# Optimization experiments

Hardware: AMD Instinct MI355X
Metric: run time of the kernel (lower is better)

The kernel has to match this reference:

```python
import jax, jax.numpy as jnp
from jax import lax
import numpy as np

EPS = 1e-6

def layer_norm(x, scale, bias):
    mu = jnp.mean(x, axis=-1, keepdims=True)
    var = jnp.var(x, axis=-1, keepdims=True)
    y = (x - mu) * lax.rsqrt(var + EPS)
    if scale is not None:
        y = y * scale
    if bias is not None:
        y = y + bias
    return y

def mha(keys, values, queries, mask, head_count):
    # keys/values: [B, K, E]; queries: [B, Q, E]; mask: [B, K] (1 = attend)
    B, Q, E = queries.shape
    d = E // head_count
    q = queries.reshape(B, Q, head_count, d) / jnp.asarray(d ** 0.5, queries.dtype)
    k = keys.reshape(B, -1, head_count, d)
    v = values.reshape(B, -1, head_count, d)
    bias = (1.0 - mask.astype(q.dtype)) * -1e12  # [B, K]
    w = jnp.einsum('bqhc,bkhc->bhqk', q, k) + bias[:, None, None, :]
    w = jax.nn.softmax(w, axis=-1)
    out = jnp.einsum('bhqk,bkhc->bqhc', w, v)
    return out.reshape(B, Q, E)

def setup_inputs() -> dict:
    key = jax.random.key(0)
    ks = jax.random.split(key, 16)
    B, T, E, G, I = 64, 64, 2048, 4096, 256
    s = 0.02
    inp = {
        'decoder_state': jax.random.normal(ks[0], (B, 1, E), jnp.float32),
        'encoder_state': jax.random.normal(ks[1], (B, T, E), jnp.float32),
        'attention_state': jnp.zeros((2 * B, I, E), jnp.float32),
        'attention_mask': jnp.ones((B, T), jnp.int32),
        'token_index': 100,
        # params
        'ln_pre_sa_b': jnp.zeros((E,), jnp.float32),
        'q_sa': s * jax.random.normal(ks[2], (E, E), jnp.float32),
        'k_sa': s * jax.random.normal(ks[3], (E, E), jnp.float32),
        'v_sa': s * jax.random.normal(ks[4], (E, E), jnp.float32),
        'o_sa': s * jax.random.normal(ks[5], (E, E), jnp.float32),
        'ln_sa_s': jnp.ones((E,), jnp.float32),
        'ln_sa_b': jnp.zeros((E,), jnp.float32),
        'ln_pre_ca_b': jnp.zeros((E,), jnp.float32),
        'q_ca': s * jax.random.normal(ks[6], (E, E), jnp.float32),
        'k_ca': s * jax.random.normal(ks[7], (E, E), jnp.float32),
        'v_ca': s * jax.random.normal(ks[8], (E, E), jnp.float32),
        'o_ca': s * jax.random.normal(ks[9], (E, E), jnp.float32),
        'ln_ca_s': jnp.ones((E,), jnp.float32),
        'ln_ca_b': jnp.zeros((E,), jnp.float32),
        'glu_ln0_b': jnp.zeros((E,), jnp.float32),
        'fc0_w': s * jax.random.normal(ks[10], (E, G), jnp.float32),
        'fc1_w': s * jax.random.normal(ks[11], (E, G), jnp.float32),
        'glu_ln1_s': jnp.ones((G,), jnp.float32),
        'glu_ln1_b': jnp.zeros((G,), jnp.float32),
        'fc2_w': s * jax.random.normal(ks[12], (G, E), jnp.float32),
    }
    return inp

IMAGE_TOKEN_COUNT = 256
HEAD_COUNT = 32

def reference(decoder_state, encoder_state, attention_state,
              ln_pre_sa_b, q_sa, k_sa, v_sa, o_sa, ln_sa_s, ln_sa_b,
              ln_pre_ca_b, q_ca, k_ca, v_ca, o_ca, ln_ca_s, ln_ca_b,
              glu_ln0_b, fc0_w, fc1_w, glu_ln1_s, glu_ln1_b, fc2_w,
              attention_mask, token_index):
    B = decoder_state.shape[0]
    # --- self attention (pre-norm, KV cache update) ---
    residual = decoder_state
    x = layer_norm(decoder_state, None, ln_pre_sa_b)
    self_mask = jnp.tile(jnp.arange(IMAGE_TOKEN_COUNT) < token_index + 1, (B, 1))
    keys = x @ k_sa
    values = x @ v_sa
    queries = x @ q_sa
    attention_state = lax.dynamic_update_slice(
        attention_state, jnp.concatenate([keys, values]).astype(jnp.float32),
        (0, token_index, 0))
    cached_k = attention_state[:B]
    cached_v = attention_state[B:]
    x = (mha(cached_k, cached_v, queries, self_mask, HEAD_COUNT) @ o_sa).astype(decoder_state.dtype)
    x = layer_norm(x, ln_sa_s, ln_sa_b)
    decoder_state = residual + x
    # --- cross attention ---
    residual = decoder_state
    x = layer_norm(decoder_state, None, ln_pre_ca_b)
    ek = encoder_state @ k_ca
    ev = encoder_state @ v_ca
    q = x @ q_ca
    x = mha(ek, ev, q, attention_mask, HEAD_COUNT) @ o_ca
    x = layer_norm(x, ln_ca_s, ln_ca_b)
    decoder_state = residual + x
    # --- GLU FFN ---
    residual = decoder_state
    z = layer_norm(decoder_state, None, glu_ln0_b)
    w = jax.nn.gelu(z @ fc0_w, approximate=False)
    v = z @ fc1_w
    z = layer_norm(w * v, glu_ln1_s, glu_ln1_b) @ fc2_w
    decoder_state = residual + z
    return decoder_state, attention_state
```

## Files before the change

### kernel.cpp

```cpp
#include <hip/hip_runtime.h>

#define Bb   64
#define Ee   2048
#define Tt   64
#define Gg   4096
#define Ii   256
#define Hh   32
#define Dd   64

using f32x4_t  = __attribute__((ext_vector_type(4))) float;
using bf16x8_t = __attribute__((ext_vector_type(8))) __bf16;

__device__ __forceinline__ unsigned short f2bf(float f) {
  unsigned u = __float_as_uint(f);
  u += 0x7FFFu + ((u >> 16) & 1u);
  return (unsigned short)(u >> 16);
}
__device__ __forceinline__ float ldkv(float v) { return v; }
__device__ __forceinline__ float ldkv(unsigned short v) {
  return __uint_as_float(((unsigned)v) << 16);
}
__device__ __forceinline__ float gelu_f(float x) {
  return 0.5f * x * (1.0f + erff(x * 0.70710678118654752f));
}

template <typename T> __device__ __forceinline__ float4 ld4(const T* p);
template <> __device__ __forceinline__ float4 ld4<float>(const float* p) {
  return *(const float4*)p;
}
template <> __device__ __forceinline__ float4 ld4<unsigned short>(const unsigned short* p) {
  ushort4 u = *(const ushort4*)p;
  return make_float4(ldkv(u.x), ldkv(u.y), ldkv(u.z), ldkv(u.w));
}

__global__ void copy_state_k(const float4* __restrict__ src, float4* __restrict__ dst,
                             const float4* __restrict__ kb, const float4* __restrict__ vb,
                             const int* __restrict__ tokp) {
  const int t = *tokp;
  const long n4 = (long)128 * Ii * (Ee / 4);
  long i = (long)blockIdx.x * blockDim.x + threadIdx.x;
  const long stride = (long)gridDim.x * blockDim.x;
  for (; i < n4; i += stride) {
    long row = i >> 9;
    int tt = (int)(row & (Ii - 1));
    float4 v;
    if (tt == t) {
      int bh  = (int)(row >> 8);
      int col = (int)(i & 511);
      const float4* s = (bh < Bb) ? kb : vb;
      v = s[(long)(bh & (Bb - 1)) * (Ee / 4) + col];
    } else {
      v = src[i];
    }
    dst[i] = v;
  }
}

__global__ void conv_bf16_k(const float4* __restrict__ in, unsigned short* __restrict__ out, long n4) {
  long i = (long)blockIdx.x * blockDim.x + threadIdx.x;
  long stride = (long)gridDim.x * blockDim.x;
  for (; i < n4; i += stride) {
    float4 f = in[i];
    ushort4 u;
    u.x = f2bf(f.x); u.y = f2bf(f.y); u.z = f2bf(f.z); u.w = f2bf(f.w);
    *(ushort4*)(out + i * 4) = u;
  }
}

__global__ void transpose_bf16_k(const float* __restrict__ W, unsigned short* __restrict__ Wt,
                                 int K, int N) {
  __shared__ unsigned short tile[64][65];
  int k0 = blockIdx.x * 64, n0 = blockIdx.y * 64;
  int c = threadIdx.x & 63;
  int r4 = threadIdx.x >> 6;
  #pragma unroll
  for (int i = 0; i < 16; i++) {
    int r = r4 + i * 4;
    tile[r][c] = f2bf(W[(long)(k0 + r) * N + n0 + c]);
  }
  __syncthreads();
  #pragma unroll
  for (int i = 0; i < 16; i++) {
    int r = r4 + i * 4;
    Wt[(long)(n0 + r) * K + k0 + c] = tile[c][r];
  }
}

template <bool GELU, bool HAS_SCALE, bool HAS_RES, bool DUAL>
__global__ void ln_k(const float4* __restrict__ in1, const float4* __restrict__ in2,
                     const float* __restrict__ scale, const float* __restrict__ bias,
                     const float4* __restrict__ res,
                     float4* __restrict__ out1, float4* __restrict__ out2) {
  const int row = blockIdx.x, tid = threadIdx.x;
  const int C = blockDim.x * 4;
  const long base = (long)row * blockDim.x + tid;

  float4 p = in1[base];
  if (GELU) {
    float4 vv = in2[base];
    p.x = gelu_f(p.x) * vv.x; p.y = gelu_f(p.y) * vv.y;
    p.z = gelu_f(p.z) * vv.z; p.w = gelu_f(p.w) * vv.w;
  }
  float s  = p.x + p.y + p.z + p.w;
  float s2 = p.x * p.x + p.y * p.y + p.z * p.z + p.w * p.w;

  __shared__ float rs[16], rs2[16];
  int lane = tid & 63, w = tid >> 6;
  #pragma unroll
  for (int o = 32; o; o >>= 1) { s += __shfl_down(s, o, 64); s2 += __shfl_down(s2, o, 64); }
  if (lane == 0) { rs[w] = s; rs2[w] = s2; }
  __syncthreads();
  if (tid == 0) {
    float ts = 0.f, ts2 = 0.f;
    int nw = blockDim.x >> 6;
    for (int i = 0; i < nw; i++) { ts += rs[i]; ts2 += rs2[i]; }
    float mu = ts / C;
    float var = ts2 / C - mu * mu;
    rs[0]  = mu;
    rs2[0] = rsqrtf(var + 1e-6f);
  }
  __syncthreads();
  const float mu = rs[0], rstd = rs2[0];

  float4 o;
  o.x = (p.x - mu) * rstd; o.y = (p.y - mu) * rstd;
  o.z = (p.z - mu) * rstd; o.w = (p.w - mu) * rstd;
  if (HAS_SCALE) {
    float4 sc4 = ((const float4*)scale)[tid];
    o.x *= sc4.x; o.y *= sc4.y; o.z *= sc4.z; o.w *= sc4.w;
  }
  float4 b4 = ((const float4*)bias)[tid];
  o.x += b4.x; o.y += b4.y; o.z += b4.z; o.w += b4.w;
  if (HAS_RES) {
    float4 r4 = res[base];
    o.x += r4.x; o.y += r4.y; o.z += r4.z; o.w += r4.w;
  }
  out1[base] = o;
  if (DUAL) out2[base] = o;
}

template <int NW>
__global__ __launch_bounds__(256)
void proj_k(const float* __restrict__ X,
            const float* __restrict__ W0, const float* __restrict__ W1,
            const float* __restrict__ W2,
            float* __restrict__ P, int K, int N) {
  __shared__ float Xs[64 * 64];
  const int nq = threadIdx.x & 31;
  const int m0 = (threadIdx.x >> 5) * 8;
  const int n  = blockIdx.x * 128 + nq * 4;
  const int kbase = blockIdx.y * 128;

  f32x4_t acc[NW][8];
  #pragma unroll
  for (int wsel = 0; wsel < NW; wsel++)
    #pragma unroll
    for (int i = 0; i < 8; i++) acc[wsel][i] = (f32x4_t){0.f, 0.f, 0.f, 0.f};

  for (int k0 = kbase; k0 < kbase + 128; k0 += 64) {
    __syncthreads();
    #pragma unroll
    for (int j = 0; j < 16; j++) {
      int e = threadIdx.x + j * 256;
      Xs[e] = X[(long)(e >> 6) * K + k0 + (e & 63)];
    }
    __syncthreads();
    #pragma unroll 4
    for (int kk = 0; kk < 64; kk++) {
      const long wrow = (long)(k0 + kk) * N + n;
      f32x4_t w4[NW];
      w4[0] = *(const f32x4_t*)(W0 + wrow);
      if (NW > 1) w4[1] = *(const f32x4_t*)(W1 + wrow);
      if (NW > 2) w4[2] = *(const f32x4_t*)(W2 + wrow);
      #pragma unroll
      for (int i = 0; i < 8; i++) {
        float xm = Xs[(m0 + i) * 64 + kk];
        #pragma unroll
        for (int wsel = 0; wsel < NW; wsel++) acc[wsel][i] += xm * w4[wsel];
      }
    }
  }
  float* base = P + (long)blockIdx.y * ((long)NW * 64 * N);
  #pragma unroll
  for (int wsel = 0; wsel < NW; wsel++) {
    #pragma unroll
    for (int i = 0; i < 8; i++) {
      *(f32x4_t*)(base + ((long)wsel * 64 + m0 + i) * N + n) = acc[wsel][i];
    }
  }
}

template <bool ACCUM>
__global__ void reduce_k(const float4* __restrict__ P, float4* __restrict__ Y,
                         int KB, long n4) {
  long i = (long)blockIdx.x * blockDim.x + threadIdx.x;
  if (i >= n4) return;
  float4 s = ACCUM ? Y[i] : make_float4(0.f, 0.f, 0.f, 0.f);
  for (int k = 0; k < KB; k++) {
    float4 p = P[(long)k * n4 + i];
    s.x += p.x; s.y += p.y; s.z += p.z; s.w += p.w;
  }
  Y[i] = s;
}

template <typename KVT>
__global__ void attn_k(const float* __restrict__ Q, const KVT* __restrict__ Kc,
                       const KVT* __restrict__ Vc, float* __restrict__ O,
                       const int* __restrict__ tokp, const int* __restrict__ maskp,
                       int L, long bstride, float scale) {
  const int b = blockIdx.x, h = blockIdx.y;
  const int lane = threadIdx.x;
  __shared__ float sc[256];
  const float* qp = Q + (long)b * Ee + h * Dd;
  const int n = tokp ? (*tokp + 1) : L;

  float mx = -3.0e38f;
  for (int pos = lane; pos < n; pos += 64) {
    bool valid = maskp ? (maskp[(long)b * L + pos] != 0) : true;
    float s = -1.0e30f;
    if (valid) {
      const KVT* kr = Kc + (long)b * bstride + (long)pos * Ee + h * Dd;
      float acc = 0.f;
      #pragma unroll
      for (int j = 0; j < 16; j++) {
        float4 kv = ld4(kr + j * 4);
        acc += qp[j*4+0]*kv.x + qp[j*4+1]*kv.y + qp[j*4+2]*kv.z + qp[j*4+3]*kv.w;
      }
      s = acc * scale;
    }
    sc[pos] = s;
    mx = fmaxf(mx, s);
  }
  __syncthreads();
  #pragma unroll
  for (int o = 32; o; o >>= 1) mx = fmaxf(mx, __shfl_down(mx, o, 64));
  mx = __shfl(mx, 0, 64);

  float sum = 0.f;
  for (int pos = lane; pos < n; pos += 64) {
    float e = expf(sc[pos] - mx);
    sc[pos] = e;
    sum += e;
  }
  __syncthreads();
  #pragma unroll
  for (int o = 32; o; o >>= 1) sum += __shfl_down(sum, o, 64);
  sum = __shfl(sum, 0, 64);
  const float inv = 1.0f / sum;

  const KVT* vbase = Vc + (long)b * bstride + h * Dd + lane;
  float acc = 0.f;
  int pos = 0;
  for (; pos + 8 <= n; pos += 8) {
    #pragma unroll
    for (int u = 0; u < 8; u++)
      acc += sc[pos + u] * ldkv(vbase[(long)(pos + u) * Ee]);
  }
  for (; pos < n; pos++) acc += sc[pos] * ldkv(vbase[(long)pos * Ee]);
  O[(long)b * Ee + h * Dd + lane] = acc * inv;
}

__global__ __launch_bounds__(256)
void gemm_bf16_k(const unsigned short* __restrict__ A, const unsigned short* __restrict__ Bt,
                 unsigned short* __restrict__ C, int M, int N, int K) {
  __shared__ unsigned short As[128 * 32];
  __shared__ unsigned short Bs[128 * 32];
  const int m0 = blockIdx.x * 128;
  const int n0 = blockIdx.y * 128;
  const int tid  = threadIdx.x;
  const int lane = tid & 63;
  const int wave = tid >> 6;
  const int wm = (wave >> 1) * 64;
  const int wn = (wave & 1) * 64;
  const int fr = lane & 15;
  const int fq = lane >> 4;

  const int r0 = tid >> 2;
  const int g0 = tid & 3;
  const int so1 = r0 * 32 + ((g0 ^ ((r0 >> 1) & 3)) * 8);
  const int so2 = so1 + 64 * 32;

  f32x4_t acc[4][4];
  const f32x4_t zero = {0.f, 0.f, 0.f, 0.f};
  #pragma unroll
  for (int i = 0; i < 4; i++)
    #pragma unroll
    for (int j = 0; j < 4; j++) acc[i][j] = zero;

  const long aR1 = (long)(m0 + r0) * K;
  const long aR2 = (long)(m0 + r0 + 64) * K;
  const long bR1 = (long)(n0 + r0) * K;
  const long bR2 = (long)(n0 + r0 + 64) * K;

  for (int k0 = 0; k0 < K; k0 += 32) {
    uint4 va1 = *(const uint4*)(A  + aR1 + k0 + g0 * 8);
    uint4 va2 = *(const uint4*)(A  + aR2 + k0 + g0 * 8);
    uint4 vb1 = *(const uint4*)(Bt + bR1 + k0 + g0 * 8);
    uint4 vb2 = *(const uint4*)(Bt + bR2 + k0 + g0 * 8);
    __syncthreads();
    *(uint4*)(As + so1) = va1;
    *(uint4*)(As + so2) = va2;
    *(uint4*)(Bs + so1) = vb1;
    *(uint4*)(Bs + so2) = vb2;
    __syncthreads();

    bf16x8_t af[4], bb[4];
    #pragma unroll
    for (int ms = 0; ms < 4; ms++) {
      int row = wm + ms * 16 + fr;
      af[ms] = __builtin_bit_cast(bf16x8_t,
               *(const uint4*)(As + row * 32 + ((fq ^ ((row >> 1) & 3)) * 8)));
    }
    #pragma unroll
    for (int ns = 0; ns < 4; ns++) {
      int row = wn + ns * 16 + fr;
      bb[ns] = __builtin_bit_cast(bf16x8_t,
               *(const uint4*)(Bs + row * 32 + ((fq ^ ((row >> 1) & 3)) * 8)));
    }
    #pragma unroll
    for (int ms = 0; ms < 4; ms++)
      #pragma unroll
      for (int ns = 0; ns < 4; ns++)
        acc[ms][ns] = __builtin_amdgcn_mfma_f32_16x16x32_bf16(af[ms], bb[ns], acc[ms][ns], 0, 0, 0);
  }

  #pragma unroll
  for (int ms = 0; ms < 4; ms++) {
    #pragma unroll
    for (int ns = 0; ns < 4; ns++) {
      int row = m0 + wm + ms * 16 + fq * 4;
      int col = n0 + wn + ns * 16 + fr;
      #pragma unroll
      for (int r = 0; r < 4; r++)
        C[(long)(row + r) * N + col] = f2bf(acc[ms][ns][r]);
    }
  }
}

extern "C" void kernel_launch(void* const* d_in, const int* in_sizes, int n_in,
                              void* d_out, int out_size, void* d_ws, size_t ws_size,
                              hipStream_t stream) {
  const float* dec    = (const float*)d_in[0];
  const float* enc    = (const float*)d_in[1];
  const float* astate = (const float*)d_in[2];
  const int*   amask  = (const int*)d_in[3];
  const int*   tokp   = (const int*)d_in[4];
  const float* ln_pre_sa_b = (const float*)d_in[5];
  const float* q_sa = (const float*)d_in[6];
  const float* k_sa = (const float*)d_in[7];
  const float* v_sa = (const float*)d_in[8];
  const float* o_sa = (const float*)d_in[9];
  const float* ln_sa_s = (const float*)d_in[10];
  const float* ln_sa_b = (const float*)d_in[11];
  const float* ln_pre_ca_b = (const float*)d_in[12];
  const float* q_ca = (const float*)d_in[13];
  const float* k_ca = (const float*)d_in[14];
  const float* v_ca = (const float*)d_in[15];
  const float* o_ca = (const float*)d_in[16];
  const float* ln_ca_s = (const float*)d_in[17];
  const float* ln_ca_b = (const float*)d_in[18];
  const float* glu_ln0_b = (const float*)d_in[19];
  const float* fc0 = (const float*)d_in[20];
  const float* fc1 = (const float*)d_in[21];
  const float* glu_ln1_s = (const float*)d_in[22];
  const float* glu_ln1_b = (const float*)d_in[23];
  const float* fc2 = (const float*)d_in[24];

  float* out_dec   = (float*)d_out;
  float* out_state = out_dec + (long)Bb * Ee;

  float* qb  = (float*)d_ws;
  float* kb  = qb  + 131072;
  float* vb  = kb  + 131072;
  float* ob  = vb  + 131072;
  float* q2  = ob  + 131072;
  float* ob2 = q2  + 131072;
  float* w0  = ob2 + 131072;
  float* v1  = w0  + 262144;
  float* x1  = v1  + 262144;
  float* ab  = x1  + 131072;
  float* ds2 = ab  + 131072;
  float* x3  = ds2 + 131072;
  float* cb  = x3  + 131072;
  float* ds3 = cb  + 131072;
  float* zb  = ds3 + 131072;
  float* wvn = zb  + 131072;
  unsigned short* ebf = (unsigned short*)(wvn + 262144);
  unsigned short* kt  = ebf + 8388608;
  unsigned short* vt  = kt  + 4194304;
  unsigned short* ekb = vt  + 4194304;
  unsigned short* evb = ekb + 8388608;
  float* arena = (float*)(evb + 8388608);

  conv_bf16_k<<<2048, 256, 0, stream>>>((const float4*)enc, ebf, (long)Bb * Tt * Ee / 4);
  transpose_bf16_k<<<dim3(32, 32), 256, 0, stream>>>(k_ca, kt, Ee, Ee);
  transpose_bf16_k<<<dim3(32, 32), 256, 0, stream>>>(v_ca, vt, Ee, Ee);
  gemm_bf16_k<<<dim3(32, 16), 256, 0, stream>>>(ebf, kt, ekb, 4096, Ee, Ee);
  gemm_bf16_k<<<dim3(32, 16), 256, 0, stream>>>(ebf, vt, evb, 4096, Ee, Ee);

  ln_k<false,false,false,false><<<Bb, 512, 0, stream>>>(
      (const float4*)dec, nullptr, nullptr, ln_pre_sa_b, nullptr, (float4*)x1, nullptr);
  proj_k<3><<<dim3(16, 16), 256, 0, stream>>>(x1, q_sa, k_sa, v_sa, arena, Ee, Ee);
  reduce_k<false><<<384, 256, 0, stream>>>((const float4*)arena, (float4*)qb, 16, 98304);
  copy_state_k<<<4096, 256, 0, stream>>>((const float4*)astate, (float4*)out_state,
                                         (const float4*)kb, (const float4*)vb, tokp);
  attn_k<float><<<dim3(Bb, Hh), 64, 0, stream>>>(qb, out_state,
      out_state + (long)Bb * Ii * Ee, ab, tokp, nullptr, Ii, (long)Ii * Ee, 0.125f);
  proj_k<1><<<dim3(16, 16), 256, 0, stream>>>(ab, o_sa, nullptr, nullptr, arena, Ee, Ee);
  reduce_k<false><<<128, 256, 0, stream>>>((const float4*)arena, (float4*)ob, 16, 32768);
  ln_k<false,true,true,false><<<Bb, 512, 0, stream>>>(
      (const float4*)ob, nullptr, ln_sa_s, ln_sa_b, (const float4*)dec, (float4*)ds2, nullptr);

  ln_k<false,false,false,false><<<Bb, 512, 0, stream>>>(
      (const float4*)ds2, nullptr, nullptr, ln_pre_ca_b, nullptr, (float4*)x3, nullptr);
  proj_k<1><<<dim3(16, 16), 256, 0, stream>>>(x3, q_ca, nullptr, nullptr, arena, Ee, Ee);
  reduce_k<false><<<128, 256, 0, stream>>>((const float4*)arena, (float4*)q2, 16, 32768);
  attn_k<unsigned short><<<dim3(Bb, Hh), 64, 0, stream>>>(q2, ekb, evb, cb,
      nullptr, amask, Tt, (long)Tt * Ee, 0.125f);
  proj_k<1><<<dim3(16, 16), 256, 0, stream>>>(cb, o_ca, nullptr, nullptr, arena, Ee, Ee);
  reduce_k<false><<<128, 256, 0, stream>>>((const float4*)arena, (float4*)ob2, 16, 32768);
  ln_k<false,true,true,true><<<Bb, 512, 0, stream>>>(
      (const float4*)ob2, nullptr, ln_ca_s, ln_ca_b, (const float4*)ds2,
      (float4*)ds3, (float4*)out_dec);

  ln_k<false,false,false,false><<<Bb, 512, 0, stream>>>(
      (const float4*)ds3, nullptr, nullptr, glu_ln0_b, nullptr, (float4*)zb, nullptr);
  proj_k<2><<<dim3(32, 16), 256, 0, stream>>>(zb, fc0, fc1, nullptr, arena, Ee, Gg);
  reduce_k<false><<<512, 256, 0, stream>>>((const float4*)arena, (float4*)w0, 16, 131072);
  ln_k<true,true,false,false><<<Bb, 1024, 0, stream>>>(
      (const float4*)w0, (const float4*)v1, glu_ln1_s, glu_ln1_b, nullptr, (float4*)wvn, nullptr);
  proj_k<1><<<dim3(16, 32), 256, 0, stream>>>(wvn, fc2, nullptr, nullptr, arena, Gg, Ee);
  reduce_k<true><<<128, 256, 0, stream>>>((const float4*)arena, (float4*)out_dec, 32, 32768);
}
```

Measured before the change: 1.072 ms.

## Reassociate cross-attention to skip encoder K/V projection GEMMs

Instead of projecting the full encoder state through k_ca and v_ca (two large 4096x2048x2048 GEMMs plus bf16 conversion and transposes), the query is first folded into k_ca per head, scores are computed directly against the raw encoder state, then probabilities weight the encoder state and the per-head context is projected through v_ca. This removes the large K/V GEMMs and bf16 staging in exchange for several smaller fp32 kernels and an extra split-K reduction. It also restores fp32 precision in the cross-attention path.

New measurement: 1.143 ms. 1.07x slower.

```diff
diff --git a/kernel.cpp b/kernel.cpp
--- a/kernel.cpp
+++ b/kernel.cpp
@@ -9,28 +9,9 @@
 #define Dd   64
 
 using f32x4_t  = __attribute__((ext_vector_type(4))) float;
-using bf16x8_t = __attribute__((ext_vector_type(8))) __bf16;
-
-__device__ __forceinline__ unsigned short f2bf(float f) {
-  unsigned u = __float_as_uint(f);
-  u += 0x7FFFu + ((u >> 16) & 1u);
-  return (unsigned short)(u >> 16);
-}
-__device__ __forceinline__ float ldkv(float v) { return v; }
-__device__ __forceinline__ float ldkv(unsigned short v) {
-  return __uint_as_float(((unsigned)v) << 16);
-}
+
 __device__ __forceinline__ float gelu_f(float x) {
   return 0.5f * x * (1.0f + erff(x * 0.70710678118654752f));
-}
-
-template <typename T> __device__ __forceinline__ float4 ld4(const T* p);
-template <> __device__ __forceinline__ float4 ld4<float>(const float* p) {
-  return *(const float4*)p;
-}
-template <> __device__ __forceinline__ float4 ld4<unsigned short>(const unsigned short* p) {
-  ushort4 u = *(const ushort4*)p;
-  return make_float4(ldkv(u.x), ldkv(u.y), ldkv(u.z), ldkv(u.w));
 }
 
 __global__ void copy_state_k(const float4* __restrict__ src, float4* __restrict__ dst,
@@ -56,36 +37,6 @@
   }
 }
 
-__global__ void conv_bf16_k(const float4* __restrict__ in, unsigned short* __restrict__ out, long n4) {
-  long i = (long)blockIdx.x * blockDim.x + threadIdx.x;
-  long stride = (long)gridDim.x * blockDim.x;
-  for (; i < n4; i += stride) {
-    float4 f = in[i];
-    ushort4 u;
-    u.x = f2bf(f.x); u.y = f2bf(f.y); u.z = f2bf(f.z); u.w = f2bf(f.w);
-    *(ushort4*)(out + i * 4) = u;
-  }
-}
-
-__global__ void transpose_bf16_k(const float* __restrict__ W, unsigned short* __restrict__ Wt,
-                                 int K, int N) {
-  __shared__ unsigned short tile[64][65];
-  int k0 = blockIdx.x * 64, n0 = blockIdx.y * 64;
-  int c = threadIdx.x & 63;
-  int r4 = threadIdx.x >> 6;
-  #pragma unroll
-  for (int i = 0; i < 16; i++) {
-    int r = r4 + i * 4;
-    tile[r][c] = f2bf(W[(long)(k0 + r) * N + n0 + c]);
-  }
-  __syncthreads();
-  #pragma unroll
-  for (int i = 0; i < 16; i++) {
-    int r = r4 + i * 4;
-    Wt[(long)(n0 + r) * K + k0 + c] = tile[c][r];
-  }
-}
-
 template <bool GELU, bool HAS_SCALE, bool HAS_RES, bool DUAL>
 __global__ void ln_k(const float4* __restrict__ in1, const float4* __restrict__ in2,
                      const float* __restrict__ scale, const float* __restrict__ bias,
@@ -203,31 +154,25 @@
   Y[i] = s;
 }
 
-template <typename KVT>
-__global__ void attn_k(const float* __restrict__ Q, const KVT* __restrict__ Kc,
-                       const KVT* __restrict__ Vc, float* __restrict__ O,
-                       const int* __restrict__ tokp, const int* __restrict__ maskp,
-                       int L, long bstride, float scale) {
+__global__ void attn_k(const float* __restrict__ Q, const float* __restrict__ Kc,
+                       const float* __restrict__ Vc, float* __restrict__ O,
+                       const int* __restrict__ tokp, int L, long bstride, float scale) {
   const int b = blockIdx.x, h = blockIdx.y;
   const int lane = threadIdx.x;
   __shared__ float sc[256];
   const float* qp = Q + (long)b * Ee + h * Dd;
-  const int n = tokp ? (*tokp + 1) : L;
+  const int n = *tokp + 1;
 
   float mx = -3.0e38f;
   for (int pos = lane; pos < n; pos += 64) {
-    bool valid = maskp ? (maskp[(long)b * L + pos] != 0) : true;
-    float s = -1.0e30f;
-    if (valid) {
-      const KVT* kr = Kc + (long)b * bstride + (long)pos * Ee + h * Dd;
-      float acc = 0.f;
-      #pragma unroll
-      for (int j = 0; j < 16; j++) {
-        float4 kv = ld4(kr + j * 4);
-        acc += qp[j*4+0]*kv.x + qp[j*4+1]*kv.y + qp[j*4+2]*kv.z + qp[j*4+3]*kv.w;
-      }
-      s = acc * scale;
-    }
+    const float* kr = Kc + (long)b * bstride + (long)pos * Ee + h * Dd;
+    float acc = 0.f;
+    #pragma unroll
+    for (int j = 0; j < 16; j++) {
+      float4 kv = *(const float4*)(kr + j * 4);
+      acc += qp[j*4+0]*kv.x + qp[j*4+1]*kv.y + qp[j*4+2]*kv.z + qp[j*4+3]*kv.w;
+    }
+    float s = acc * scale;
     sc[pos] = s;
     mx = fmaxf(mx, s);
   }
@@ -248,93 +193,173 @@
   sum = __shfl(sum, 0, 64);
   const float inv = 1.0f / sum;
 
-  const KVT* vbase = Vc + (long)b * bstride + h * Dd + lane;
+  const float* vbase = Vc + (long)b * bstride + h * Dd + lane;
   float acc = 0.f;
   int pos = 0;
   for (; pos + 8 <= n; pos += 8) {
     #pragma unroll
     for (int u = 0; u < 8; u++)
-      acc += sc[pos + u] * ldkv(vbase[(long)(pos + u) * Ee]);
-  }
-  for (; pos < n; pos++) acc += sc[pos] * ldkv(vbase[(long)pos * Ee]);
+      acc += sc[pos + u] * vbase[(long)(pos + u) * Ee];
+  }
+  for (; pos < n; pos++) acc += sc[pos] * vbase[(long)pos * Ee];
   O[(long)b * Ee + h * Dd + lane] = acc * inv;
 }
 
+
 __global__ __launch_bounds__(256)
-void gemm_bf16_k(const unsigned short* __restrict__ A, const unsigned short* __restrict__ Bt,
-                 unsigned short* __restrict__ C, int M, int N, int K) {
-  __shared__ unsigned short As[128 * 32];
-  __shared__ unsigned short Bs[128 * 32];
-  const int m0 = blockIdx.x * 128;
-  const int n0 = blockIdx.y * 128;
-  const int tid  = threadIdx.x;
-  const int lane = tid & 63;
-  const int wave = tid >> 6;
-  const int wm = (wave >> 1) * 64;
-  const int wn = (wave & 1) * 64;
-  const int fr = lane & 15;
-  const int fq = lane >> 4;
-
-  const int r0 = tid >> 2;
-  const int g0 = tid & 3;
-  const int so1 = r0 * 32 + ((g0 ^ ((r0 >> 1) & 3)) * 8);
-  const int so2 = so1 + 64 * 32;
-
-  f32x4_t acc[4][4];
-  const f32x4_t zero = {0.f, 0.f, 0.f, 0.f};
+void headA_k(const float* __restrict__ Q, const float* __restrict__ Kca,
+             float* __restrict__ A) {
+  const int h  = blockIdx.x;
+  const int e0 = blockIdx.y * 128;
+  __shared__ float Qs[64][64];
+  __shared__ float Kt[64][132];
+  const int tid = threadIdx.x;
+
+  #pragma unroll
+  for (int j = 0; j < 16; j++) {
+    int idx = tid + j * 256;
+    Qs[idx >> 6][idx & 63] = Q[(long)(idx >> 6) * Ee + h * 64 + (idx & 63)];
+  }
+  #pragma unroll
+  for (int j = 0; j < 32; j++) {
+    int idx = tid + j * 256;
+    int r = idx >> 6, c = idx & 63;
+    Kt[c][r] = Kca[(long)(e0 + r) * Ee + h * 64 + c];
+  }
+  __syncthreads();
+
+  const int nq = tid & 31, m0 = (tid >> 5) * 8;
+  f32x4_t acc[8];
+  #pragma unroll
+  for (int i = 0; i < 8; i++) acc[i] = (f32x4_t){0.f, 0.f, 0.f, 0.f};
+  #pragma unroll 8
+  for (int c = 0; c < 64; c++) {
+    f32x4_t w4 = *(const f32x4_t*)&Kt[c][nq * 4];
+    #pragma unroll
+    for (int i = 0; i < 8; i++) acc[i] += Qs[m0 + i][c] * w4;
+  }
+  #pragma unroll
+  for (int i = 0; i < 8; i++)
+    *(f32x4_t*)&A[((long)(m0 + i) * Hh + h) * Ee + e0 + nq * 4] = acc[i] * 0.125f;
+}
+
+__global__ __launch_bounds__(256)
+void sm_k(const float* __restrict__ A, const float* __restrict__ enc,
+          const int* __restrict__ mask, float* __restrict__ P) {
+  const int b = blockIdx.x, hg = blockIdx.y;
+  __shared__ float Es[64][65];
+  __shared__ float As[8][64];
+  const int tid = threadIdx.x;
+  const int t = tid & 63, h2 = tid >> 6;
+
+  float s0 = 0.f, s1 = 0.f;
+  for (int e0 = 0; e0 < Ee; e0 += 64) {
+    __syncthreads();
+    #pragma unroll
+    for (int j = 0; j < 16; j++) {
+      int idx = tid + j * 256;
+      Es[idx >> 6][idx & 63] = enc[((long)b * Tt + (idx >> 6)) * Ee + e0 + (idx & 63)];
+    }
+    #pragma unroll
+    for (int j = 0; j < 2; j++) {
+      int idx = tid + j * 256;
+      As[idx >> 6][idx & 63] =
+          A[((long)b * Hh + hg * 8 + (idx >> 6)) * Ee + e0 + (idx & 63)];
+    }
+    __syncthreads();
+    #pragma unroll 8
+    for (int e = 0; e < 64; e++) {
+      float es = Es[t][e];
+      s0 += As[h2][e] * es;
+      s1 += As[h2 + 4][e] * es;
+    }
+  }
+
+  if (mask[(long)b * Tt + t] == 0) { s0 = -1e30f; s1 = -1e30f; }
+  float m0v = s0, m1v = s1;
+  #pragma unroll
+  for (int o = 32; o; o >>= 1) {
+    m0v = fmaxf(m0v, __shfl_xor(m0v, o, 64));
+    m1v = fmaxf(m1v, __shfl_xor(m1v, o, 64));
+  }
+  float p0 = expf(s0 - m0v), p1 = expf(s1 - m1v);
+  float d0 = p0, d1 = p1;
+  #pragma unroll
+  for (int o = 32; o; o >>= 1) {
+    d0 += __shfl_xor(d0, o, 64);
+    d1 += __shfl_xor(d1, o, 64);
+  }
+  P[((long)b * Hh + hg * 8 + h2) * Tt + t]     = p0 / d0;
+  P[((long)b * Hh + hg * 8 + h2 + 4) * Tt + t] = p1 / d1;
+}
+
+__global__ __launch_bounds__(256)
+void ctxB_k(const float* __restrict__ P, const float* __restrict__ enc,
+            float* __restrict__ C) {
+  const int b = blockIdx.x, e0 = blockIdx.y * 256;
+  __shared__ float Ps[32][64];
+  const int tid = threadIdx.x;
+  #pragma unroll
+  for (int j = 0; j < 8; j++) {
+    int idx = tid + j * 256;
+    Ps[idx >> 6][idx & 63] = P[(long)b * (Hh * Tt) + idx];
+  }
+  __syncthreads();
+
+  float acc[32];
+  #pragma unroll
+  for (int h = 0; h < 32; h++) acc[h] = 0.f;
+  const float* ep = enc + (long)b * Tt * Ee + e0 + tid;
+  for (int t0 = 0; t0 < Tt; t0 += 4) {
+    float ev0 = ep[(long)(t0 + 0) * Ee];
+    float ev1 = ep[(long)(t0 + 1) * Ee];
+    float ev2 = ep[(long)(t0 + 2) * Ee];
+    float ev3 = ep[(long)(t0 + 3) * Ee];
+    #pragma unroll
+    for (int h = 0; h < 32; h++) {
+      f32x4_t p4 = *(const f32x4_t*)&Ps[h][t0];
+      acc[h] += p4[0] * ev0 + p4[1] * ev1 + p4[2] * ev2 + p4[3] * ev3;
+    }
+  }
+  #pragma unroll
+  for (int h = 0; h < 32; h++)
+    C[((long)b * Hh + h) * Ee + e0 + tid] = acc[h];
+}
+
+__global__ __launch_bounds__(256)
+void ctxC_k(const float* __restrict__ C, const float* __restrict__ Vca,
+            float* __restrict__ Pout) {
+  const int h  = blockIdx.x;
+  const int kb = blockIdx.y;
+  __shared__ float Xs[64][65];
+  __shared__ float Ws[64][64];
+  const int tid = threadIdx.x;
+  const int nq = tid & 15, m0 = (tid >> 4) * 4;
+
+  f32x4_t acc[4];
+  #pragma unroll
+  for (int i = 0; i < 4; i++) acc[i] = (f32x4_t){0.f, 0.f, 0.f, 0.f};
+
+  for (int k0 = kb * 512; k0 < kb * 512 + 512; k0 += 64) {
+    __syncthreads();
+    #pragma unroll
+    for (int j = 0; j < 16; j++) {
+      int idx = tid + j * 256;
+      int r = idx >> 6, cc = idx & 63;
+      Xs[r][cc] = C[((long)r * Hh + h) * Ee + k0 + cc];
+      Ws[r][cc] = Vca[(long)(k0 + r) * Ee + h * 64 + cc];
+    }
+    __syncthreads();
+    #pragma unroll 4
+    for (int kk = 0; kk < 64; kk++) {
+      f32x4_t w4 = *(const f32x4_t*)&Ws[kk][nq * 4];
+      #pragma unroll
+      for (int i = 0; i < 4; i++) acc[i] += Xs[m0 + i][kk] * w4;
+    }
+  }
   #pragma unroll
   for (int i = 0; i < 4; i++)
-    #pragma unroll
-    for (int j = 0; j < 4; j++) acc[i][j] = zero;
-
-  const long aR1 = (long)(m0 + r0) * K;
-  const long aR2 = (long)(m0 + r0 + 64) * K;
-  const long bR1 = (long)(n0 + r0) * K;
-  const long bR2 = (long)(n0 + r0 + 64) * K;
-
-  for (int k0 = 0; k0 < K; k0 += 32) {
-    uint4 va1 = *(const uint4*)(A  + aR1 + k0 + g0 * 8);
-    uint4 va2 = *(const uint4*)(A  + aR2 + k0 + g0 * 8);
-    uint4 vb1 = *(const uint4*)(Bt + bR1 + k0 + g0 * 8);
-    uint4 vb2 = *(const uint4*)(Bt + bR2 + k0 + g0 * 8);
-    __syncthreads();
-    *(uint4*)(As + so1) = va1;
-    *(uint4*)(As + so2) = va2;
-    *(uint4*)(Bs + so1) = vb1;
-    *(uint4*)(Bs + so2) = vb2;
-    __syncthreads();
-
-    bf16x8_t af[4], bb[4];
-    #pragma unroll
-    for (int ms = 0; ms < 4; ms++) {
-      int row = wm + ms * 16 + fr;
-      af[ms] = __builtin_bit_cast(bf16x8_t,
-               *(const uint4*)(As + row * 32 + ((fq ^ ((row >> 1) & 3)) * 8)));
-    }
-    #pragma unroll
-    for (int ns = 0; ns < 4; ns++) {
-      int row = wn + ns * 16 + fr;
-      bb[ns] = __builtin_bit_cast(bf16x8_t,
-               *(const uint4*)(Bs + row * 32 + ((fq ^ ((row >> 1) & 3)) * 8)));
-    }
-    #pragma unroll
-    for (int ms = 0; ms < 4; ms++)
-      #pragma unroll
-      for (int ns = 0; ns < 4; ns++)
-        acc[ms][ns] = __builtin_amdgcn_mfma_f32_16x16x32_bf16(af[ms], bb[ns], acc[ms][ns], 0, 0, 0);
-  }
-
-  #pragma unroll
-  for (int ms = 0; ms < 4; ms++) {
-    #pragma unroll
-    for (int ns = 0; ns < 4; ns++) {
-      int row = m0 + wm + ms * 16 + fq * 4;
-      int col = n0 + wn + ns * 16 + fr;
-      #pragma unroll
-      for (int r = 0; r < 4; r++)
-        C[(long)(row + r) * N + col] = f2bf(acc[ms][ns][r]);
-    }
-  }
+    *(f32x4_t*)&Pout[((long)kb * 64 + m0 + i) * Ee + h * 64 + nq * 4] = acc[i];
 }
 
 extern "C" void kernel_launch(void* const* d_in, const int* in_sizes, int n_in,
@@ -385,18 +410,10 @@
   float* ds3 = cb  + 131072;
   float* zb  = ds3 + 131072;
   float* wvn = zb  + 131072;
-  unsigned short* ebf = (unsigned short*)(wvn + 262144);
-  unsigned short* kt  = ebf + 8388608;
-  unsigned short* vt  = kt  + 4194304;
-  unsigned short* ekb = vt  + 4194304;
-  unsigned short* evb = ekb + 8388608;
-  float* arena = (float*)(evb + 8388608);
-
-  conv_bf16_k<<<2048, 256, 0, stream>>>((const float4*)enc, ebf, (long)Bb * Tt * Ee / 4);
-  transpose_bf16_k<<<dim3(32, 32), 256, 0, stream>>>(k_ca, kt, Ee, Ee);
-  transpose_bf16_k<<<dim3(32, 32), 256, 0, stream>>>(v_ca, vt, Ee, Ee);
-  gemm_bf16_k<<<dim3(32, 16), 256, 0, stream>>>(ebf, kt, ekb, 4096, Ee, Ee);
-  gemm_bf16_k<<<dim3(32, 16), 256, 0, stream>>>(ebf, vt, evb, 4096, Ee, Ee);
+  float* Ab   = wvn + 262144;
+  float* ctxb = Ab  + 4194304;
+  float* Pb   = ctxb + 4194304;
+  float* arena = Pb + 131072;
 
   ln_k<false,false,false,false><<<Bb, 512, 0, stream>>>(
       (const float4*)dec, nullptr, nullptr, ln_pre_sa_b, nullptr, (float4*)x1, nullptr);
@@ -404,8 +421,8 @@
   reduce_k<false><<<384, 256, 0, stream>>>((const float4*)arena, (float4*)qb, 16, 98304);
   copy_state_k<<<4096, 256, 0, stream>>>((const float4*)astate, (float4*)out_state,
                                          (const float4*)kb, (const float4*)vb, tokp);
-  attn_k<float><<<dim3(Bb, Hh), 64, 0, stream>>>(qb, out_state,
-      out_state + (long)Bb * Ii * Ee, ab, tokp, nullptr, Ii, (long)Ii * Ee, 0.125f);
+  attn_k<<<dim3(Bb, Hh), 64, 0, stream>>>(qb, out_state,
+      out_state + (long)Bb * Ii * Ee, ab, tokp, Ii, (long)Ii * Ee, 0.125f);
   proj_k<1><<<dim3(16, 16), 256, 0, stream>>>(ab, o_sa, nullptr, nullptr, arena, Ee, Ee);
   reduce_k<false><<<128, 256, 0, stream>>>((const float4*)arena, (float4*)ob, 16, 32768);
   ln_k<false,true,true,false><<<Bb, 512, 0, stream>>>(
@@ -415,8 +432,11 @@
       (const float4*)ds2, nullptr, nullptr, ln_pre_ca_b, nullptr, (float4*)x3, nullptr);
   proj_k<1><<<dim3(16, 16), 256, 0, stream>>>(x3, q_ca, nullptr, nullptr, arena, Ee, Ee);
   reduce_k<false><<<128, 256, 0, stream>>>((const float4*)arena, (float4*)q2, 16, 32768);
-  attn_k<unsigned short><<<dim3(Bb, Hh), 64, 0, stream>>>(q2, ekb, evb, cb,
-      nullptr, amask, Tt, (long)Tt * Ee, 0.125f);
+  headA_k<<<dim3(Hh, 16), 256, 0, stream>>>(q2, k_ca, Ab);
+  sm_k<<<dim3(Bb, 4), 256, 0, stream>>>(Ab, enc, amask, Pb);
+  ctxB_k<<<dim3(Bb, 8), 256, 0, stream>>>(Pb, enc, ctxb);
+  ctxC_k<<<dim3(Hh, 4), 256, 0, stream>>>(ctxb, v_ca, arena);
+  reduce_k<false><<<128, 256, 0, stream>>>((const float4*)arena, (float4*)cb, 4, 32768);
   proj_k<1><<<dim3(16, 16), 256, 0, stream>>>(cb, o_ca, nullptr, nullptr, arena, Ee, Ee);
   reduce_k<false><<<128, 256, 0, stream>>>((const float4*)arena, (float4*)ob2, 16, 32768);
   ln_k<false,true,true,true><<<Bb, 512, 0, stream>>>(
```
